# Performance work log

Hardware: AMD Instinct MI355X
Metric: run time of the kernel (lower is better)

Reference implementation:

```python
import jax, jax.numpy as jnp
import numpy as np

B, L, D_SEQ, D_GLOBAL = 32, 2048, 1024, 1024
H, DK, DV = 16, 64, 64


def setup_inputs() -> dict:
    key = jax.random.key(0)
    k1, k2, k3, k4, k5 = jax.random.split(key, 5)
    scale = 0.05
    return {
        "X": jax.random.normal(k1, (B, D_GLOBAL), dtype=jnp.float32),
        "S": jax.random.normal(k2, (B, L, D_SEQ), dtype=jnp.float32),
        "Wq": jax.random.normal(k3, (H, D_GLOBAL, DK), dtype=jnp.float32) * scale,
        "Wk": jax.random.normal(k4, (H, D_SEQ, DK), dtype=jnp.float32) * scale,
        "Wv": jax.random.normal(k5, (H, D_SEQ, DV), dtype=jnp.float32) * scale,
    }


def reference(X, S, Wq, Wk, Wv):
    # X: [B, d_global], S: [B, L, d_seq]
    d_key = Wq.shape[-1]
    inv_sqrt_dk = 1.0 / jnp.sqrt(jnp.float32(d_key))
    # Values: gelu (exact, erf-based like tf default) projection -> [B, H, L, DV]
    VS = jax.nn.gelu(jnp.einsum("bld,hdv->bhlv", S, Wv), approximate=False)
    # Single global query per head: tanh projection -> [B, H, DK]
    Q = jnp.tanh(jnp.einsum("bd,hdk->bhk", X, Wq))
    # Keys: tanh projection -> [B, H, L, DK]
    KS = jnp.tanh(jnp.einsum("bld,hdk->bhlk", S, Wk))
    # Attention logits (batched GEMV): [B, H, L]
    logits = jnp.einsum("bhk,bhlk->bhl", Q, KS) * inv_sqrt_dk
    Z = jax.nn.softmax(logits, axis=-1)
    # Weighted sum of values: [B, H, DV] -> flatten to [B, H*DV]
    Y = jnp.einsum("bhl,bhlv->bhv", Z, VS)
    return Y.reshape(Y.shape[0], -1)
```

## Files before the change

### kernel.cpp

```cpp
#include <hip/hip_runtime.h>
#include <math.h>

#define B_   32
#define L_   2048
#define DSEQ 1024
#define DGLB 1024
#define H_   16
#define DK_  64
#define DV_  64
#define LT   64
#define NT   (L_/LT)
#define PSTRIDE 66

#define WC_KSTRIDE 4096
#define WC_HSTRIDE 131072

#define AS1 __attribute__((address_space(1)))
#define AS3 __attribute__((address_space(3)))

using u16    = unsigned short;
using bf16x8 = __attribute__((ext_vector_type(8))) short;
using f32x4  = __attribute__((ext_vector_type(4))) float;

__device__ __forceinline__ u16 f2bf(float x) {
  union { float f; unsigned int u; } v; v.f = x;
  return (u16)((v.u + 0x7fffu + ((v.u >> 16) & 1u)) >> 16);
}

__device__ __forceinline__ float tanh_fast(float x) {
  float e = __builtin_exp2f(x * 2.885390081777927f);
  return 1.f - 2.f/(e + 1.f);
}

__device__ __forceinline__ float erf_fast(float x) {
  float ax = fabsf(x);
  float t  = 1.f/(1.f + 0.3275911f*ax);
  float p  = t*(0.254829592f + t*(-0.284496736f + t*(1.421413741f +
             t*(-1.453152027f + t*1.061405429f))));
  float e  = __builtin_exp2f(-ax*ax*1.4426950408889634f);
  float r  = 1.f - p*e;
  return copysignf(r, x);
}

#define PHASE_BARRIER(N)                                   \
  do {                                                     \
    __builtin_amdgcn_sched_barrier(0);                     \
    asm volatile("s_waitcnt vmcnt(" #N ")" ::: "memory");  \
    __builtin_amdgcn_s_barrier();                          \
    __builtin_amdgcn_sched_barrier(0);                     \
  } while (0)

__global__ void pack_w_kernel(const float* __restrict__ Wk,
                              const float* __restrict__ Wv,
                              u16* __restrict__ Wc) {
  const int h = blockIdx.x, j = blockIdx.y;
  const float* src = (j < DK_) ? (Wk + (size_t)h*DSEQ*DK_ + j)
                               : (Wv + (size_t)h*DSEQ*DV_ + (j - DK_));
  u16* dst = Wc + (size_t)h*WC_HSTRIDE + (size_t)j*32;
  for (int d = threadIdx.x; d < DSEQ; d += blockDim.x)
    dst[(size_t)(d >> 5)*WC_KSTRIDE + (d & 31)] = f2bf(src[(size_t)d*64]);
}

__global__ void s2bf_kernel(const float* __restrict__ S, u16* __restrict__ Sb) {
  const size_t G = (size_t)B_*L_*DSEQ/8;
  for (size_t i = (size_t)blockIdx.x*256 + threadIdx.x; i < G; i += (size_t)4096*256) {
    const float4* sp = (const float4*)(S + i*8);
    float4 v0 = sp[0], v1 = sp[1];
    bf16x8 wv;
    wv[0]=(short)f2bf(v0.x); wv[1]=(short)f2bf(v0.y);
    wv[2]=(short)f2bf(v0.z); wv[3]=(short)f2bf(v0.w);
    wv[4]=(short)f2bf(v1.x); wv[5]=(short)f2bf(v1.y);
    wv[6]=(short)f2bf(v1.z); wv[7]=(short)f2bf(v1.w);
    *(bf16x8*)(Sb + i*8) = wv;
  }
}

__global__ void q_proj_kernel(const float* __restrict__ X,
                              const float* __restrict__ Wq,
                              float* __restrict__ Q) {
  const int h = blockIdx.x, b0 = blockIdx.y*4, k = threadIdx.x;
  const float* w = Wq + (size_t)h*DGLB*DK_ + k;
  float a0=0.f, a1=0.f, a2=0.f, a3=0.f;
  for (int d = 0; d < DGLB; ++d) {
    float wv = w[(size_t)d*DK_];
    a0 += X[(size_t)(b0+0)*DGLB + d]*wv;
    a1 += X[(size_t)(b0+1)*DGLB + d]*wv;
    a2 += X[(size_t)(b0+2)*DGLB + d]*wv;
    a3 += X[(size_t)(b0+3)*DGLB + d]*wv;
  }
  Q[((size_t)(b0+0)*H_+h)*DK_+k] = tanhf(a0);
  Q[((size_t)(b0+1)*H_+h)*DK_+k] = tanhf(a1);
  Q[((size_t)(b0+2)*H_+h)*DK_+k] = tanhf(a2);
  Q[((size_t)(b0+3)*H_+h)*DK_+k] = tanhf(a3);
}

template<int BF16SRC>
__global__ __launch_bounds__(256, 3) void fused_kernel(
    const float* __restrict__ S, const u16* __restrict__ Sb,
    const u16* __restrict__ Wc, const float* __restrict__ Q,
    float* __restrict__ part) {
  __shared__ u16   Slds[3*64*128];
  __shared__ float lpart[2][64];

  const int id   = blockIdx.x;
  const int slot = id & 7;
  const int m    = id >> 3;
  const int tile = (m + (slot << 7)) & 1023;
  const int t    = tile & (NT-1), b = tile >> 5;

  const int tid  = threadIdx.x;
  const int wave = tid >> 6, lane = tid & 63;
  const int lhi  = lane >> 4, llo = lane & 15;
  const int isV  = wave & 1,  hp  = wave >> 1;
  const int h    = slot*2 + hp;

  const u16* wb = Wc + (size_t)h*WC_HSTRIDE + (size_t)(isV*64 + llo)*32 + lhi*8;
  int arow[4];
  #pragma unroll
  for (int rt = 0; rt < 4; ++rt) arow[rt] = (rt*16 + llo)*256;

  const u16*   Sv = Sb + ((size_t)b*L_ + (size_t)t*LT)*DSEQ;
  const float* Sf = S  + ((size_t)b*L_ + (size_t)t*LT)*DSEQ;

  auto stage_gl = [&](int sub) {
    const int bs = (sub % 3) * 8192;
    #pragma unroll
    for (int it = 0; it < 4; ++it) {
      const int j   = wave*4 + it;
      const int row = 4*j + (lane >> 4);
      const int g   = (lane & 15) ^ (row & 15);
      const u16* gp = Sv + (size_t)row*DSEQ + sub*128 + (g << 3);
      __builtin_amdgcn_global_load_lds(
          (const AS1 void*)gp, (AS3 void*)(Slds + bs + j*512), 16, 0, 0);
    }
  };
  auto stage_reg = [&](int sub) {
    const int bs = (sub % 3) * 16384;
    #pragma unroll
    for (int it = 0; it < 4; ++it) {
      int f = it*256 + tid, row = f >> 4, q = f & 15;
      int g = q ^ (row & 15);
      const float4* sp = (const float4*)(Sf + (size_t)row*DSEQ + sub*128 + g*8);
      float4 v0 = sp[0], v1 = sp[1];
      bf16x8 wv;
      wv[0]=(short)f2bf(v0.x); wv[1]=(short)f2bf(v0.y);
      wv[2]=(short)f2bf(v0.z); wv[3]=(short)f2bf(v0.w);
      wv[4]=(short)f2bf(v1.x); wv[5]=(short)f2bf(v1.y);
      wv[6]=(short)f2bf(v1.z); wv[7]=(short)f2bf(v1.w);
      *(bf16x8*)((char*)Slds + bs + row*256 + q*16) = wv;
    }
  };

  f32x4 acc[4][4];
  #pragma unroll
  for (int rt = 0; rt < 4; ++rt)
    #pragma unroll
    for (int c = 0; c < 4; ++c) acc[rt][c] = {0.f,0.f,0.f,0.f};

  if (BF16SRC) {
    stage_gl(0);
    stage_gl(1);
    __builtin_amdgcn_sched_barrier(0);
  }
  bf16x8 bA[4], bB[4], bC[4], bD[4];
  #pragma unroll
  for (int c = 0; c < 4; ++c) bA[c] = *(const bf16x8*)(wb + (size_t)0*WC_KSTRIDE + c*512);
  #pragma unroll
  for (int c = 0; c < 4; ++c) bB[c] = *(const bf16x8*)(wb + (size_t)1*WC_KSTRIDE + c*512);
  #pragma unroll
  for (int c = 0; c < 4; ++c) bC[c] = *(const bf16x8*)(wb + (size_t)2*WC_KSTRIDE + c*512);
  #pragma unroll
  for (int c = 0; c < 4; ++c) bD[c] = *(const bf16x8*)(wb + (size_t)3*WC_KSTRIDE + c*512);
  const u16* wbp = wb + (size_t)4*WC_KSTRIDE;
  if (BF16SRC) PHASE_BARRIER(20);

#define KSTEP(BUF, kk)                                                        \
  do {                                                                        \
    const int colb = (((kk)*4 + lhi) ^ llo) << 4;                             \
    __builtin_amdgcn_s_setprio(1);                                            \
    _Pragma("unroll")                                                         \
    for (int rt = 0; rt < 4; ++rt) {                                          \
      bf16x8 af = *(const bf16x8*)(cb + arow[rt] + colb);                     \
      acc[rt][0] = __builtin_amdgcn_mfma_f32_16x16x32_bf16(af, BUF[0], acc[rt][0], 0,0,0); \
      acc[rt][1] = __builtin_amdgcn_mfma_f32_16x16x32_bf16(af, BUF[1], acc[rt][1], 0,0,0); \
      acc[rt][2] = __builtin_amdgcn_mfma_f32_16x16x32_bf16(af, BUF[2], acc[rt][2], 0,0,0); \
      acc[rt][3] = __builtin_amdgcn_mfma_f32_16x16x32_bf16(af, BUF[3], acc[rt][3], 0,0,0); \
    }                                                                         \
    __builtin_amdgcn_s_setprio(0);                                            \
    _Pragma("unroll")                                                         \
    for (int c = 0; c < 4; ++c)                                               \
      BUF[c] = *(const bf16x8*)(wbp + c*512);                                 \
    wbp += ((s*4 + (kk) + 4) == 31) ? -(ptrdiff_t)(31*WC_KSTRIDE)             \
                                    : (ptrdiff_t)WC_KSTRIDE;                  \
  } while (0)

  #pragma unroll
  for (int s = 0; s < 8; ++s) {
    if (BF16SRC) {
      if (s < 6) { stage_gl(s + 2); __builtin_amdgcn_sched_barrier(0); }
    } else {
      stage_reg(s);
      __syncthreads();
    }
    const char* cb = (const char*)Slds + (s % 3)*16384;
    KSTEP(bA, 0); KSTEP(bB, 1); KSTEP(bC, 2); KSTEP(bD, 3);
    if (BF16SRC) {
      if (s < 6)       PHASE_BARRIER(36);
      else if (s == 6) PHASE_BARRIER(32);
    } else {
      __syncthreads();
    }
  }
#undef KSTEP

  if (!isV) {
    const float* Qb = Q + ((size_t)b*H_ + h)*DK_;
    float q[4];
    #pragma unroll
    for (int c = 0; c < 4; ++c) q[c] = Qb[16*c + llo];
    #pragma unroll
    for (int rt = 0; rt < 4; ++rt) {
      #pragma unroll
      for (int r = 0; r < 4; ++r) {
        float pl = q[0]*tanh_fast(acc[rt][0][r]) + q[1]*tanh_fast(acc[rt][1][r])
                 + q[2]*tanh_fast(acc[rt][2][r]) + q[3]*tanh_fast(acc[rt][3][r]);
        pl += __shfl_xor(pl, 1); pl += __shfl_xor(pl, 2);
        pl += __shfl_xor(pl, 4); pl += __shfl_xor(pl, 8);
        if (llo == 0) lpart[hp][rt*16 + lhi*4 + r] = pl;
      }
    }
  } else {
    #pragma unroll
    for (int rt = 0; rt < 4; ++rt)
      #pragma unroll
      for (int c = 0; c < 4; ++c)
        #pragma unroll
        for (int r = 0; r < 4; ++r) {
          float x = acc[rt][c][r];
          acc[rt][c][r] = 0.5f*x*(1.f + erf_fast(x*0.70710678118654752f));
        }
  }
  __syncthreads();

  if (isV) {
    float lg = lpart[hp][lane] * 0.125f;
    float mx = lg;
    #pragma unroll
    for (int mk = 1; mk < 64; mk <<= 1) mx = fmaxf(mx, __shfl_xor(mx, mk));
    float ev = __expf(lg - mx);
    float sv = ev;
    #pragma unroll
    for (int mk = 1; mk < 64; mk <<= 1) sv += __shfl_xor(sv, mk);

    float er[16];
    #pragma unroll
    for (int rt = 0; rt < 4; ++rt)
      #pragma unroll
      for (int r = 0; r < 4; ++r)
        er[rt*4 + r] = __shfl(ev, rt*16 + lhi*4 + r);

    float* pt = part + (((size_t)b*H_ + h)*NT + t)*PSTRIDE;
    #pragma unroll
    for (int c = 0; c < 4; ++c) {
      float y = 0.f;
      #pragma unroll
      for (int rt = 0; rt < 4; ++rt)
        #pragma unroll
        for (int r = 0; r < 4; ++r)
          y += er[rt*4 + r]*acc[rt][c][r];
      y += __shfl_xor(y, 16); y += __shfl_xor(y, 32);
      if (lhi == 0) pt[2 + 16*c + llo] = y;
    }
    if (lane == 0) { pt[0] = mx; pt[1] = sv; }
  }
}

__global__ void finalize_kernel(const float* __restrict__ part,
                                float* __restrict__ out) {
  const int h = blockIdx.x, b = blockIdx.y, v = threadIdx.x;
  const float* p = part + ((size_t)b*H_ + h)*(size_t)NT*PSTRIDE;
  float M = -3.0e38f;
  for (int tt = 0; tt < NT; ++tt) M = fmaxf(M, p[tt*PSTRIDE]);
  float ss = 0.f, y = 0.f;
  for (int tt = 0; tt < NT; ++tt) {
    float w = expf(p[tt*PSTRIDE] - M);
    ss += w*p[tt*PSTRIDE + 1];
    y  += w*p[tt*PSTRIDE + 2 + v];
  }
  out[((size_t)b*H_ + h)*DV_ + v] = y/ss;
}

extern "C" void kernel_launch(void* const* d_in, const int* in_sizes, int n_in,
                              void* d_out, int out_size, void* d_ws, size_t ws_size,
                              hipStream_t stream) {
  const float* X  = (const float*)d_in[0];
  const float* S  = (const float*)d_in[1];
  const float* Wq = (const float*)d_in[2];
  const float* Wk = (const float*)d_in[3];
  const float* Wv = (const float*)d_in[4];
  float* out = (float*)d_out;

  char* ws = (char*)d_ws;
  u16*   Wc    = (u16*)ws;
  float* Qbuf  = (float*)(ws + (4u<<20));
  float* part  = (float*)(ws + (4u<<20) + (128u<<10));
  u16*   Sb    = (u16*)(ws + (16u<<20));
  const bool useBf = ws_size >= (144ull << 20);

  pack_w_kernel  <<<dim3(H_, 128),  256, 0, stream>>>(Wk, Wv, Wc);
  q_proj_kernel  <<<dim3(H_, B_/4),  64, 0, stream>>>(X, Wq, Qbuf);
  if (useBf) {
    s2bf_kernel         <<<dim3(4096), 256, 0, stream>>>(S, Sb);
    fused_kernel<1>     <<<dim3(NT*B_*8), 256, 0, stream>>>(S, Sb, Wc, Qbuf, part);
  } else {
    fused_kernel<0>     <<<dim3(NT*B_*8), 256, 0, stream>>>(S, Sb, Wc, Qbuf, part);
  }
  finalize_kernel<<<dim3(H_, B_),    64, 0, stream>>>(part, out);
}
```

Measured before the change: 460.8 us.

## Enlarge fused GEMM tile to 128 rows with LDS-staged weights and 512 threads

The fused projection kernel now processes 128 sequence rows per block with 8 waves (two M-halves by four head/K-V column groups) instead of 64 rows with 4 waves. Weights are repacked into a new layout and staged through LDS alongside S in a triple-buffered 64-wide K pipeline, rather than streamed from global memory into registers per wave. The aim is to halve redundant weight traffic per S row and raise MFMA reuse per LDS load. In exchange the kernel uses more LDS per block, runs more barrier phases, and occupancy drops to two 512-thread blocks per CU.

```diff
diff --git a/kernel.cpp b/kernel.cpp
--- a/kernel.cpp
+++ b/kernel.cpp
@@ -8,12 +8,9 @@
 #define H_   16
 #define DK_  64
 #define DV_  64
-#define LT   64
-#define NT   (L_/LT)
+#define NT   32
 #define PSTRIDE 66
 
-#define WC_KSTRIDE 4096
-#define WC_HSTRIDE 131072
 
 #define AS1 __attribute__((address_space(1)))
 #define AS3 __attribute__((address_space(3)))
@@ -56,9 +53,11 @@
   const int h = blockIdx.x, j = blockIdx.y;
   const float* src = (j < DK_) ? (Wk + (size_t)h*DSEQ*DK_ + j)
                                : (Wv + (size_t)h*DSEQ*DV_ + (j - DK_));
-  u16* dst = Wc + (size_t)h*WC_HSTRIDE + (size_t)j*32;
-  for (int d = threadIdx.x; d < DSEQ; d += blockDim.x)
-    dst[(size_t)(d >> 5)*WC_KSTRIDE + (d & 31)] = f2bf(src[(size_t)d*64]);
+  for (int d = threadIdx.x; d < DSEQ; d += blockDim.x) {
+    int kt = d >> 6, ks = (d >> 5) & 1, lh = (d >> 3) & 3, e = d & 7;
+    Wc[(size_t)(h*128 + kt*8 + ks*4 + lh)*1024 + j*8 + e] =
+        f2bf(src[(size_t)d*64]);
+  }
 }
 
 __global__ void s2bf_kernel(const float* __restrict__ S, u16* __restrict__ Sb) {
@@ -95,59 +94,80 @@
 }
 
 template<int BF16SRC>
-__global__ __launch_bounds__(256, 3) void fused_kernel(
+__global__ __launch_bounds__(512, 2) void fused_kernel(
     const float* __restrict__ S, const u16* __restrict__ Sb,
     const u16* __restrict__ Wc, const float* __restrict__ Q,
     float* __restrict__ part) {
-  __shared__ u16   Slds[3*64*128];
-  __shared__ float lpart[2][64];
-
-  const int id   = blockIdx.x;
-  const int slot = id & 7;
-  const int m    = id >> 3;
-  const int tile = (m + (slot << 7)) & 1023;
-  const int t    = tile & (NT-1), b = tile >> 5;
+  __shared__ u16   Slds[3*24576];
+  __shared__ float lpart[2][2][64];
+
+  const int id    = blockIdx.x;
+  const int slot  = id & 7;
+  const int Mtile = ((id >> 3) + (slot << 6)) & 511;
+  const int b     = Mtile >> 4;
+  const int rowb  = (Mtile & 15) * 128;
 
   const int tid  = threadIdx.x;
   const int wave = tid >> 6, lane = tid & 63;
   const int lhi  = lane >> 4, llo = lane & 15;
-  const int isV  = wave & 1,  hp  = wave >> 1;
+  const int mw   = wave & 1,  nv  = wave >> 1;
+  const int hp   = nv >> 1,   isV = nv & 1;
   const int h    = slot*2 + hp;
 
-  const u16* wb = Wc + (size_t)h*WC_HSTRIDE + (size_t)(isV*64 + llo)*32 + lhi*8;
-  int arow[4];
-  #pragma unroll
-  for (int rt = 0; rt < 4; ++rt) arow[rt] = (rt*16 + llo)*256;
-
-  const u16*   Sv = Sb + ((size_t)b*L_ + (size_t)t*LT)*DSEQ;
-  const float* Sf = S  + ((size_t)b*L_ + (size_t)t*LT)*DSEQ;
-
-  auto stage_gl = [&](int sub) {
-    const int bs = (sub % 3) * 8192;
+  const u16* Sv = Sb + ((size_t)b*L_ + rowb)*DSEQ;
+  const float* Sf = S + ((size_t)b*L_ + rowb)*DSEQ;
+  const u16* Wh = Wc + (size_t)slot*2*131072;
+
+  auto stage_gl = [&](int sub, int p) {
+    u16* Ab = Slds + p*24576;
+    u16* Bb = Ab + 8192;
+    #pragma unroll
+    for (int it = 0; it < 2; ++it) {
+      const int j   = wave*2 + it;
+      const int row = 8*j + (lane >> 3);
+      const int g   = (lane & 7) ^ (row & 7);
+      const u16* gp = Sv + (size_t)row*DSEQ + sub*64 + g*8;
+      __builtin_amdgcn_global_load_lds(
+          (const AS1 void*)gp, (AS3 void*)(Ab + j*512), 16, 0, 0);
+    }
     #pragma unroll
     for (int it = 0; it < 4; ++it) {
-      const int j   = wave*4 + it;
-      const int row = 4*j + (lane >> 4);
-      const int g   = (lane & 15) ^ (row & 15);
-      const u16* gp = Sv + (size_t)row*DSEQ + sub*128 + (g << 3);
+      const int c  = wave*4 + it;
+      const int ks = c >> 4, lh = (c >> 2) & 3, jg = c & 3;
+      const int col = jg*64 + lane;
+      const u16* gp = Wh + (size_t)((col >> 7)*128 + sub*8 + ks*4 + lh)*1024
+                         + (size_t)(col & 127)*8;
       __builtin_amdgcn_global_load_lds(
-          (const AS1 void*)gp, (AS3 void*)(Slds + bs + j*512), 16, 0, 0);
+          (const AS1 void*)gp,
+          (AS3 void*)(Bb + ((ks*4 + lh)*256 + jg*64)*8), 16, 0, 0);
     }
   };
-  auto stage_reg = [&](int sub) {
-    const int bs = (sub % 3) * 16384;
-    #pragma unroll
-    for (int it = 0; it < 4; ++it) {
-      int f = it*256 + tid, row = f >> 4, q = f & 15;
-      int g = q ^ (row & 15);
-      const float4* sp = (const float4*)(Sf + (size_t)row*DSEQ + sub*128 + g*8);
+  auto stage_reg = [&](int sub, int p) {
+    u16* Ab = Slds + p*24576;
+    u16* Bb = Ab + 8192;
+    #pragma unroll
+    for (int it = 0; it < 2; ++it) {
+      const int j   = wave*2 + it;
+      const int row = 8*j + (lane >> 3);
+      const int g   = (lane & 7) ^ (row & 7);
+      const float4* sp = (const float4*)(Sf + (size_t)row*DSEQ + sub*64 + g*8);
       float4 v0 = sp[0], v1 = sp[1];
       bf16x8 wv;
       wv[0]=(short)f2bf(v0.x); wv[1]=(short)f2bf(v0.y);
       wv[2]=(short)f2bf(v0.z); wv[3]=(short)f2bf(v0.w);
       wv[4]=(short)f2bf(v1.x); wv[5]=(short)f2bf(v1.y);
       wv[6]=(short)f2bf(v1.z); wv[7]=(short)f2bf(v1.w);
-      *(bf16x8*)((char*)Slds + bs + row*256 + q*16) = wv;
+      *(bf16x8*)(Ab + j*512 + lane*8) = wv;
+    }
+    #pragma unroll
+    for (int it = 0; it < 4; ++it) {
+      const int c  = wave*4 + it;
+      const int ks = c >> 4, lh = (c >> 2) & 3, jg = c & 3;
+      const int col = jg*64 + lane;
+      const u16* gp = Wh + (size_t)((col >> 7)*128 + sub*8 + ks*4 + lh)*1024
+                         + (size_t)(col & 127)*8;
+      bf16x8 wv = *(const bf16x8*)gp;
+      *(bf16x8*)(Bb + ((ks*4 + lh)*256 + jg*64)*8 + lane*8) = wv;
     }
   };
 
@@ -158,60 +178,55 @@
     for (int c = 0; c < 4; ++c) acc[rt][c] = {0.f,0.f,0.f,0.f};
 
   if (BF16SRC) {
-    stage_gl(0);
-    stage_gl(1);
-    __builtin_amdgcn_sched_barrier(0);
-  }
-  bf16x8 bA[4], bB[4], bC[4], bD[4];
-  #pragma unroll
-  for (int c = 0; c < 4; ++c) bA[c] = *(const bf16x8*)(wb + (size_t)0*WC_KSTRIDE + c*512);
-  #pragma unroll
-  for (int c = 0; c < 4; ++c) bB[c] = *(const bf16x8*)(wb + (size_t)1*WC_KSTRIDE + c*512);
-  #pragma unroll
-  for (int c = 0; c < 4; ++c) bC[c] = *(const bf16x8*)(wb + (size_t)2*WC_KSTRIDE + c*512);
-  #pragma unroll
-  for (int c = 0; c < 4; ++c) bD[c] = *(const bf16x8*)(wb + (size_t)3*WC_KSTRIDE + c*512);
-  const u16* wbp = wb + (size_t)4*WC_KSTRIDE;
-  if (BF16SRC) PHASE_BARRIER(20);
-
-#define KSTEP(BUF, kk)                                                        \
-  do {                                                                        \
-    const int colb = (((kk)*4 + lhi) ^ llo) << 4;                             \
-    __builtin_amdgcn_s_setprio(1);                                            \
-    _Pragma("unroll")                                                         \
-    for (int rt = 0; rt < 4; ++rt) {                                          \
-      bf16x8 af = *(const bf16x8*)(cb + arow[rt] + colb);                     \
-      acc[rt][0] = __builtin_amdgcn_mfma_f32_16x16x32_bf16(af, BUF[0], acc[rt][0], 0,0,0); \
-      acc[rt][1] = __builtin_amdgcn_mfma_f32_16x16x32_bf16(af, BUF[1], acc[rt][1], 0,0,0); \
-      acc[rt][2] = __builtin_amdgcn_mfma_f32_16x16x32_bf16(af, BUF[2], acc[rt][2], 0,0,0); \
-      acc[rt][3] = __builtin_amdgcn_mfma_f32_16x16x32_bf16(af, BUF[3], acc[rt][3], 0,0,0); \
-    }                                                                         \
-    __builtin_amdgcn_s_setprio(0);                                            \
-    _Pragma("unroll")                                                         \
-    for (int c = 0; c < 4; ++c)                                               \
-      BUF[c] = *(const bf16x8*)(wbp + c*512);                                 \
-    wbp += ((s*4 + (kk) + 4) == 31) ? -(ptrdiff_t)(31*WC_KSTRIDE)             \
-                                    : (ptrdiff_t)WC_KSTRIDE;                  \
-  } while (0)
-
-  #pragma unroll
-  for (int s = 0; s < 8; ++s) {
+    stage_gl(0, 0);
+    stage_gl(1, 1);
+    PHASE_BARRIER(6);
+  } else {
+    stage_reg(0, 0);
+    stage_reg(1, 1);
+    __syncthreads();
+  }
+
+  const int arow0 = mw*64 + llo;
+  const int llo7  = llo & 7;
+
+  int p = 0;
+  for (int s = 0; s < 16; ++s) {
+    const int pn = (p == 2) ? 0 : p + 1;
+    const int p2 = (pn == 2) ? 0 : pn + 1;
+    if (s < 14) {
+      if (BF16SRC) { stage_gl(s + 2, p2); __builtin_amdgcn_sched_barrier(0); }
+      else         { stage_reg(s + 2, p2); }
+    }
+    const u16* Ab = Slds + p*24576;
+    const u16* Bb = Ab + 8192;
+    #pragma unroll
+    for (int kk = 0; kk < 2; ++kk) {
+      const u16* Bp = Bb + ((kk*4 + lhi)*256 + nv*64 + llo)*8;
+      bf16x8 b0 = *(const bf16x8*)(Bp);
+      bf16x8 b1 = *(const bf16x8*)(Bp + 128);
+      bf16x8 b2 = *(const bf16x8*)(Bp + 256);
+      bf16x8 b3 = *(const bf16x8*)(Bp + 384);
+      const int sl = ((kk*4 + lhi) ^ llo7)*8;
+      __builtin_amdgcn_s_setprio(1);
+      #pragma unroll
+      for (int rt = 0; rt < 4; ++rt) {
+        bf16x8 af = *(const bf16x8*)(Ab + (arow0 + rt*16)*64 + sl);
+        acc[rt][0] = __builtin_amdgcn_mfma_f32_16x16x32_bf16(af, b0, acc[rt][0], 0,0,0);
+        acc[rt][1] = __builtin_amdgcn_mfma_f32_16x16x32_bf16(af, b1, acc[rt][1], 0,0,0);
+        acc[rt][2] = __builtin_amdgcn_mfma_f32_16x16x32_bf16(af, b2, acc[rt][2], 0,0,0);
+        acc[rt][3] = __builtin_amdgcn_mfma_f32_16x16x32_bf16(af, b3, acc[rt][3], 0,0,0);
+      }
+      __builtin_amdgcn_s_setprio(0);
+    }
     if (BF16SRC) {
-      if (s < 6) { stage_gl(s + 2); __builtin_amdgcn_sched_barrier(0); }
-    } else {
-      stage_reg(s);
-      __syncthreads();
-    }
-    const char* cb = (const char*)Slds + (s % 3)*16384;
-    KSTEP(bA, 0); KSTEP(bB, 1); KSTEP(bC, 2); KSTEP(bD, 3);
-    if (BF16SRC) {
-      if (s < 6)       PHASE_BARRIER(36);
-      else if (s == 6) PHASE_BARRIER(32);
+      if (s < 14)       PHASE_BARRIER(6);
+      else if (s == 14) PHASE_BARRIER(0);
     } else {
       __syncthreads();
     }
-  }
-#undef KSTEP
+    p = pn;
+  }
 
   if (!isV) {
     const float* Qb = Q + ((size_t)b*H_ + h)*DK_;
@@ -226,7 +241,7 @@
                  + q[2]*tanh_fast(acc[rt][2][r]) + q[3]*tanh_fast(acc[rt][3][r]);
         pl += __shfl_xor(pl, 1); pl += __shfl_xor(pl, 2);
         pl += __shfl_xor(pl, 4); pl += __shfl_xor(pl, 8);
-        if (llo == 0) lpart[hp][rt*16 + lhi*4 + r] = pl;
+        if (llo == 0) lpart[mw][hp][rt*16 + lhi*4 + r] = pl;
       }
     }
   } else {
@@ -243,7 +258,7 @@
   __syncthreads();
 
   if (isV) {
-    float lg = lpart[hp][lane] * 0.125f;
+    float lg = lpart[mw][hp][lane] * 0.125f;
     float mx = lg;
     #pragma unroll
     for (int mk = 1; mk < 64; mk <<= 1) mx = fmaxf(mx, __shfl_xor(mx, mk));
@@ -259,7 +274,8 @@
       for (int r = 0; r < 4; ++r)
         er[rt*4 + r] = __shfl(ev, rt*16 + lhi*4 + r);
 
-    float* pt = part + (((size_t)b*H_ + h)*NT + t)*PSTRIDE;
+    const int t_local = (Mtile & 15)*2 + mw;
+    float* pt = part + (((size_t)b*H_ + h)*NT + t_local)*PSTRIDE;
     #pragma unroll
     for (int c = 0; c < 4; ++c) {
       float y = 0.f;
@@ -310,10 +326,10 @@
   pack_w_kernel  <<<dim3(H_, 128),  256, 0, stream>>>(Wk, Wv, Wc);
   q_proj_kernel  <<<dim3(H_, B_/4),  64, 0, stream>>>(X, Wq, Qbuf);
   if (useBf) {
-    s2bf_kernel         <<<dim3(4096), 256, 0, stream>>>(S, Sb);
-    fused_kernel<1>     <<<dim3(NT*B_*8), 256, 0, stream>>>(S, Sb, Wc, Qbuf, part);
+    s2bf_kernel       <<<dim3(4096), 256, 0, stream>>>(S, Sb);
+    fused_kernel<1>   <<<dim3(4096), 512, 0, stream>>>(S, Sb, Wc, Qbuf, part);
   } else {
-    fused_kernel<0>     <<<dim3(NT*B_*8), 256, 0, stream>>>(S, Sb, Wc, Qbuf, part);
+    fused_kernel<0>   <<<dim3(4096), 512, 0, stream>>>(S, Sb, Wc, Qbuf, part);
   }
   finalize_kernel<<<dim3(H_, B_),    64, 0, stream>>>(part, out);
 }
```

After: 621.5 us. 1.35x slower.

## Process four heads per block in two passes to halve block count

Applied to the files above, without the earlier changes.

Each block now handles four heads (two per pass) over the same S tile instead of two, so the grid shrinks from 8192 to 4096 blocks. The S tile is streamed through LDS twice, but the W prefetch and LDS pipeline continue across the pass boundary, and setup and launch overhead are amortized over more work. The intent is to cut per-block fixed costs and improve locality of the S tile in cache. The cost is a longer serial chain per block, fewer blocks to balance across CUs, and the S tile still being reloaded from global or L2 in the second pass.

```diff
diff --git a/kernel.cpp b/kernel.cpp
--- a/kernel.cpp
+++ b/kernel.cpp
@@ -104,17 +104,16 @@
 
   const int id   = blockIdx.x;
   const int slot = id & 7;
+  const int grp  = slot >> 1;
   const int m    = id >> 3;
-  const int tile = (m + (slot << 7)) & 1023;
+  const int tile = (((m + (grp << 7)) & 511) << 1) | (slot & 1);
   const int t    = tile & (NT-1), b = tile >> 5;
 
   const int tid  = threadIdx.x;
   const int wave = tid >> 6, lane = tid & 63;
   const int lhi  = lane >> 4, llo = lane & 15;
   const int isV  = wave & 1,  hp  = wave >> 1;
-  const int h    = slot*2 + hp;
-
-  const u16* wb = Wc + (size_t)h*WC_HSTRIDE + (size_t)(isV*64 + llo)*32 + lhi*8;
+
   int arow[4];
   #pragma unroll
   for (int rt = 0; rt < 4; ++rt) arow[rt] = (rt*16 + llo)*256;
@@ -124,23 +123,25 @@
 
   auto stage_gl = [&](int sub) {
     const int bs = (sub % 3) * 8192;
+    const int ko = (sub & 7) * 128;
     #pragma unroll
     for (int it = 0; it < 4; ++it) {
       const int j   = wave*4 + it;
       const int row = 4*j + (lane >> 4);
       const int g   = (lane & 15) ^ (row & 15);
-      const u16* gp = Sv + (size_t)row*DSEQ + sub*128 + (g << 3);
+      const u16* gp = Sv + (size_t)row*DSEQ + ko + (g << 3);
       __builtin_amdgcn_global_load_lds(
           (const AS1 void*)gp, (AS3 void*)(Slds + bs + j*512), 16, 0, 0);
     }
   };
   auto stage_reg = [&](int sub) {
     const int bs = (sub % 3) * 16384;
+    const int ko = (sub & 7) * 128;
     #pragma unroll
     for (int it = 0; it < 4; ++it) {
       int f = it*256 + tid, row = f >> 4, q = f & 15;
       int g = q ^ (row & 15);
-      const float4* sp = (const float4*)(Sf + (size_t)row*DSEQ + sub*128 + g*8);
+      const float4* sp = (const float4*)(Sf + (size_t)row*DSEQ + ko + g*8);
       float4 v0 = sp[0], v1 = sp[1];
       bf16x8 wv;
       wv[0]=(short)f2bf(v0.x); wv[1]=(short)f2bf(v0.y);
@@ -151,12 +152,8 @@
     }
   };
 
-  f32x4 acc[4][4];
-  #pragma unroll
-  for (int rt = 0; rt < 4; ++rt)
-    #pragma unroll
-    for (int c = 0; c < 4; ++c) acc[rt][c] = {0.f,0.f,0.f,0.f};
-
+  const u16* wb = Wc + (size_t)(grp*4 + hp)*WC_HSTRIDE
+                     + (size_t)(isV*64 + llo)*32 + lhi*8;
   if (BF16SRC) {
     stage_gl(0);
     stage_gl(1);
@@ -190,89 +187,102 @@
     _Pragma("unroll")                                                         \
     for (int c = 0; c < 4; ++c)                                               \
       BUF[c] = *(const bf16x8*)(wbp + c*512);                                 \
-    wbp += ((s*4 + (kk) + 4) == 31) ? -(ptrdiff_t)(31*WC_KSTRIDE)             \
-                                    : (ptrdiff_t)WC_KSTRIDE;                  \
+    wbp += ((s8*4 + (kk) + 4) == 31) ? wrapjump : (ptrdiff_t)WC_KSTRIDE;      \
   } while (0)
 
-  #pragma unroll
-  for (int s = 0; s < 8; ++s) {
-    if (BF16SRC) {
-      if (s < 6) { stage_gl(s + 2); __builtin_amdgcn_sched_barrier(0); }
-    } else {
-      stage_reg(s);
-      __syncthreads();
-    }
-    const char* cb = (const char*)Slds + (s % 3)*16384;
-    KSTEP(bA, 0); KSTEP(bB, 1); KSTEP(bC, 2); KSTEP(bD, 3);
-    if (BF16SRC) {
-      if (s < 6)       PHASE_BARRIER(36);
-      else if (s == 6) PHASE_BARRIER(32);
-    } else {
-      __syncthreads();
-    }
-  }
-#undef KSTEP
-
-  if (!isV) {
-    const float* Qb = Q + ((size_t)b*H_ + h)*DK_;
-    float q[4];
-    #pragma unroll
-    for (int c = 0; c < 4; ++c) q[c] = Qb[16*c + llo];
-    #pragma unroll
-    for (int rt = 0; rt < 4; ++rt) {
-      #pragma unroll
-      for (int r = 0; r < 4; ++r) {
-        float pl = q[0]*tanh_fast(acc[rt][0][r]) + q[1]*tanh_fast(acc[rt][1][r])
-                 + q[2]*tanh_fast(acc[rt][2][r]) + q[3]*tanh_fast(acc[rt][3][r]);
-        pl += __shfl_xor(pl, 1); pl += __shfl_xor(pl, 2);
-        pl += __shfl_xor(pl, 4); pl += __shfl_xor(pl, 8);
-        if (llo == 0) lpart[hp][rt*16 + lhi*4 + r] = pl;
-      }
-    }
-  } else {
+  for (int pass = 0; pass < 2; ++pass) {
+    const int h = grp*4 + pass*2 + hp;
+    const ptrdiff_t wrapjump = (pass == 0)
+        ? (ptrdiff_t)2*WC_HSTRIDE - (ptrdiff_t)31*WC_KSTRIDE
+        : -(ptrdiff_t)31*WC_KSTRIDE;
+
+    f32x4 acc[4][4];
     #pragma unroll
     for (int rt = 0; rt < 4; ++rt)
       #pragma unroll
-      for (int c = 0; c < 4; ++c)
+      for (int c = 0; c < 4; ++c) acc[rt][c] = {0.f,0.f,0.f,0.f};
+
+    #pragma unroll
+    for (int s8 = 0; s8 < 8; ++s8) {
+      const int sg = pass*8 + s8;
+      if (BF16SRC) {
+        if (sg <= 13) { stage_gl(sg + 2); __builtin_amdgcn_sched_barrier(0); }
+      } else {
+        stage_reg(sg);
+        __syncthreads();
+      }
+      const char* cb = (const char*)Slds + (sg % 3)*16384;
+      KSTEP(bA, 0); KSTEP(bB, 1); KSTEP(bC, 2); KSTEP(bD, 3);
+      if (BF16SRC) {
+        if (sg <= 13)       PHASE_BARRIER(36);
+        else if (sg == 14)  PHASE_BARRIER(32);
+      } else {
+        __syncthreads();
+      }
+    }
+
+    if (!isV) {
+      const float* Qb = Q + ((size_t)b*H_ + h)*DK_;
+      float q[4];
+      #pragma unroll
+      for (int c = 0; c < 4; ++c) q[c] = Qb[16*c + llo];
+      #pragma unroll
+      for (int rt = 0; rt < 4; ++rt) {
         #pragma unroll
         for (int r = 0; r < 4; ++r) {
-          float x = acc[rt][c][r];
-          acc[rt][c][r] = 0.5f*x*(1.f + erf_fast(x*0.70710678118654752f));
+          float pl = q[0]*tanh_fast(acc[rt][0][r]) + q[1]*tanh_fast(acc[rt][1][r])
+                   + q[2]*tanh_fast(acc[rt][2][r]) + q[3]*tanh_fast(acc[rt][3][r]);
+          pl += __shfl_xor(pl, 1); pl += __shfl_xor(pl, 2);
+          pl += __shfl_xor(pl, 4); pl += __shfl_xor(pl, 8);
+          if (llo == 0) lpart[hp][rt*16 + lhi*4 + r] = pl;
         }
-  }
-  __syncthreads();
-
-  if (isV) {
-    float lg = lpart[hp][lane] * 0.125f;
-    float mx = lg;
-    #pragma unroll
-    for (int mk = 1; mk < 64; mk <<= 1) mx = fmaxf(mx, __shfl_xor(mx, mk));
-    float ev = __expf(lg - mx);
-    float sv = ev;
-    #pragma unroll
-    for (int mk = 1; mk < 64; mk <<= 1) sv += __shfl_xor(sv, mk);
-
-    float er[16];
-    #pragma unroll
-    for (int rt = 0; rt < 4; ++rt)
-      #pragma unroll
-      for (int r = 0; r < 4; ++r)
-        er[rt*4 + r] = __shfl(ev, rt*16 + lhi*4 + r);
-
-    float* pt = part + (((size_t)b*H_ + h)*NT + t)*PSTRIDE;
-    #pragma unroll
-    for (int c = 0; c < 4; ++c) {
-      float y = 0.f;
+      }
+    } else {
+      #pragma unroll
+      for (int rt = 0; rt < 4; ++rt)
+        #pragma unroll
+        for (int c = 0; c < 4; ++c)
+          #pragma unroll
+          for (int r = 0; r < 4; ++r) {
+            float x = acc[rt][c][r];
+            acc[rt][c][r] = 0.5f*x*(1.f + erf_fast(x*0.70710678118654752f));
+          }
+    }
+    __syncthreads();
+
+    if (isV) {
+      float lg = lpart[hp][lane] * 0.125f;
+      float mx = lg;
+      #pragma unroll
+      for (int mk = 1; mk < 64; mk <<= 1) mx = fmaxf(mx, __shfl_xor(mx, mk));
+      float ev = __expf(lg - mx);
+      float sv = ev;
+      #pragma unroll
+      for (int mk = 1; mk < 64; mk <<= 1) sv += __shfl_xor(sv, mk);
+
+      float er[16];
       #pragma unroll
       for (int rt = 0; rt < 4; ++rt)
         #pragma unroll
         for (int r = 0; r < 4; ++r)
-          y += er[rt*4 + r]*acc[rt][c][r];
-      y += __shfl_xor(y, 16); y += __shfl_xor(y, 32);
-      if (lhi == 0) pt[2 + 16*c + llo] = y;
-    }
-    if (lane == 0) { pt[0] = mx; pt[1] = sv; }
-  }
+          er[rt*4 + r] = __shfl(ev, rt*16 + lhi*4 + r);
+
+      float* pt = part + (((size_t)b*H_ + h)*NT + t)*PSTRIDE;
+      #pragma unroll
+      for (int c = 0; c < 4; ++c) {
+        float y = 0.f;
+        #pragma unroll
+        for (int rt = 0; rt < 4; ++rt)
+          #pragma unroll
+          for (int r = 0; r < 4; ++r)
+            y += er[rt*4 + r]*acc[rt][c][r];
+        y += __shfl_xor(y, 16); y += __shfl_xor(y, 32);
+        if (lhi == 0) pt[2 + 16*c + llo] = y;
+      }
+      if (lane == 0) { pt[0] = mx; pt[1] = sv; }
+    }
+  }
+#undef KSTEP
 }
 
 __global__ void finalize_kernel(const float* __restrict__ part,
@@ -310,10 +320,10 @@
   pack_w_kernel  <<<dim3(H_, 128),  256, 0, stream>>>(Wk, Wv, Wc);
   q_proj_kernel  <<<dim3(H_, B_/4),  64, 0, stream>>>(X, Wq, Qbuf);
   if (useBf) {
-    s2bf_kernel         <<<dim3(4096), 256, 0, stream>>>(S, Sb);
-    fused_kernel<1>     <<<dim3(NT*B_*8), 256, 0, stream>>>(S, Sb, Wc, Qbuf, part);
+    s2bf_kernel       <<<dim3(4096), 256, 0, stream>>>(S, Sb);
+    fused_kernel<1>   <<<dim3(4096), 256, 0, stream>>>(S, Sb, Wc, Qbuf, part);
   } else {
-    fused_kernel<0>     <<<dim3(NT*B_*8), 256, 0, stream>>>(S, Sb, Wc, Qbuf, part);
+    fused_kernel<0>   <<<dim3(4096), 256, 0, stream>>>(S, Sb, Wc, Qbuf, part);
   }
   finalize_kernel<<<dim3(H_, B_),    64, 0, stream>>>(part, out);
 }
```

Measured after the change: 657.3 us. 1.43x slower.

## Retile fused kernel to one head per block with 128-row L tiles

Applied to the files above, without the earlier changes.

Changes the work split so each block handles one head over 128 sequence rows instead of two heads over 64 rows. The four waves now split the K/V output columns (32 each) and stream K in 64-wide chunks over 16 stages. Logit partial sums from two waves are combined in LDS before the softmax. The aim is to halve redundant S-tile loads per head pair and balance per-wave B-fragment loads. The cost is more pipeline stages with smaller MFMA work per stage and different register pressure.

```diff
diff --git a/kernel.cpp b/kernel.cpp
--- a/kernel.cpp
+++ b/kernel.cpp
@@ -8,8 +8,7 @@
 #define H_   16
 #define DK_  64
 #define DV_  64
-#define LT   64
-#define NT   (L_/LT)
+#define NT   32
 #define PSTRIDE 66
 
 #define WC_KSTRIDE 4096
@@ -99,141 +98,140 @@
     const float* __restrict__ S, const u16* __restrict__ Sb,
     const u16* __restrict__ Wc, const float* __restrict__ Q,
     float* __restrict__ part) {
-  __shared__ u16   Slds[3*64*128];
-  __shared__ float lpart[2][64];
+  __shared__ u16   Slds[3*8192];
+  __shared__ float lpart[2][128];
 
   const int id   = blockIdx.x;
-  const int slot = id & 7;
-  const int m    = id >> 3;
-  const int tile = (m + (slot << 7)) & 1023;
-  const int t    = tile & (NT-1), b = tile >> 5;
+  const int head = id & 15;
+  const int m    = id >> 4;
+  const int tile = (m + (head << 5)) & 511;
+  const int b    = tile >> 4, t2 = tile & 15;
 
   const int tid  = threadIdx.x;
   const int wave = tid >> 6, lane = tid & 63;
   const int lhi  = lane >> 4, llo = lane & 15;
-  const int isV  = wave & 1,  hp  = wave >> 1;
-  const int h    = slot*2 + hp;
-
-  const u16* wb = Wc + (size_t)h*WC_HSTRIDE + (size_t)(isV*64 + llo)*32 + lhi*8;
-  int arow[4];
-  #pragma unroll
-  for (int rt = 0; rt < 4; ++rt) arow[rt] = (rt*16 + llo)*256;
-
-  const u16*   Sv = Sb + ((size_t)b*L_ + (size_t)t*LT)*DSEQ;
-  const float* Sf = S  + ((size_t)b*L_ + (size_t)t*LT)*DSEQ;
+  const int llo7 = llo & 7;
+
+  int arow[8];
+  #pragma unroll
+  for (int rt = 0; rt < 8; ++rt) arow[rt] = (rt*16 + llo)*128;
+
+  const u16*   Sv = Sb + ((size_t)b*L_ + (size_t)t2*128)*DSEQ;
+  const float* Sf = S  + ((size_t)b*L_ + (size_t)t2*128)*DSEQ;
 
   auto stage_gl = [&](int sub) {
     const int bs = (sub % 3) * 8192;
+    const int ko = sub * 64;
     #pragma unroll
     for (int it = 0; it < 4; ++it) {
       const int j   = wave*4 + it;
-      const int row = 4*j + (lane >> 4);
-      const int g   = (lane & 15) ^ (row & 15);
-      const u16* gp = Sv + (size_t)row*DSEQ + sub*128 + (g << 3);
+      const int row = 8*j + (lane >> 3);
+      const int g   = (lane & 7) ^ (row & 7);
+      const u16* gp = Sv + (size_t)row*DSEQ + ko + (g << 3);
       __builtin_amdgcn_global_load_lds(
           (const AS1 void*)gp, (AS3 void*)(Slds + bs + j*512), 16, 0, 0);
     }
   };
   auto stage_reg = [&](int sub) {
     const int bs = (sub % 3) * 16384;
+    const int ko = sub * 64;
     #pragma unroll
     for (int it = 0; it < 4; ++it) {
-      int f = it*256 + tid, row = f >> 4, q = f & 15;
-      int g = q ^ (row & 15);
-      const float4* sp = (const float4*)(Sf + (size_t)row*DSEQ + sub*128 + g*8);
+      int f = it*256 + tid, row = f >> 3, q = f & 7;
+      int g = q ^ (row & 7);
+      const float4* sp = (const float4*)(Sf + (size_t)row*DSEQ + ko + g*8);
       float4 v0 = sp[0], v1 = sp[1];
       bf16x8 wv;
       wv[0]=(short)f2bf(v0.x); wv[1]=(short)f2bf(v0.y);
       wv[2]=(short)f2bf(v0.z); wv[3]=(short)f2bf(v0.w);
       wv[4]=(short)f2bf(v1.x); wv[5]=(short)f2bf(v1.y);
       wv[6]=(short)f2bf(v1.z); wv[7]=(short)f2bf(v1.w);
-      *(bf16x8*)((char*)Slds + bs + row*256 + q*16) = wv;
+      *(bf16x8*)((char*)Slds + bs + row*128 + q*16) = wv;
     }
   };
 
-  f32x4 acc[4][4];
-  #pragma unroll
-  for (int rt = 0; rt < 4; ++rt)
-    #pragma unroll
-    for (int c = 0; c < 4; ++c) acc[rt][c] = {0.f,0.f,0.f,0.f};
-
+  f32x4 acc[8][2];
+  #pragma unroll
+  for (int rt = 0; rt < 8; ++rt) {
+    acc[rt][0] = {0.f,0.f,0.f,0.f};
+    acc[rt][1] = {0.f,0.f,0.f,0.f};
+  }
+
+  const u16* wb = Wc + (size_t)head*WC_HSTRIDE
+                     + (size_t)(wave*32 + llo)*32 + lhi*8;
   if (BF16SRC) {
     stage_gl(0);
     stage_gl(1);
     __builtin_amdgcn_sched_barrier(0);
   }
-  bf16x8 bA[4], bB[4], bC[4], bD[4];
-  #pragma unroll
-  for (int c = 0; c < 4; ++c) bA[c] = *(const bf16x8*)(wb + (size_t)0*WC_KSTRIDE + c*512);
-  #pragma unroll
-  for (int c = 0; c < 4; ++c) bB[c] = *(const bf16x8*)(wb + (size_t)1*WC_KSTRIDE + c*512);
-  #pragma unroll
-  for (int c = 0; c < 4; ++c) bC[c] = *(const bf16x8*)(wb + (size_t)2*WC_KSTRIDE + c*512);
-  #pragma unroll
-  for (int c = 0; c < 4; ++c) bD[c] = *(const bf16x8*)(wb + (size_t)3*WC_KSTRIDE + c*512);
+  bf16x8 bA[2], bB[2], bC[2], bD[2];
+  #pragma unroll
+  for (int c = 0; c < 2; ++c) bA[c] = *(const bf16x8*)(wb + (size_t)0*WC_KSTRIDE + c*512);
+  #pragma unroll
+  for (int c = 0; c < 2; ++c) bB[c] = *(const bf16x8*)(wb + (size_t)1*WC_KSTRIDE + c*512);
+  #pragma unroll
+  for (int c = 0; c < 2; ++c) bC[c] = *(const bf16x8*)(wb + (size_t)2*WC_KSTRIDE + c*512);
+  #pragma unroll
+  for (int c = 0; c < 2; ++c) bD[c] = *(const bf16x8*)(wb + (size_t)3*WC_KSTRIDE + c*512);
   const u16* wbp = wb + (size_t)4*WC_KSTRIDE;
-  if (BF16SRC) PHASE_BARRIER(20);
+  if (BF16SRC) PHASE_BARRIER(12);
 
 #define KSTEP(BUF, kk)                                                        \
   do {                                                                        \
-    const int colb = (((kk)*4 + lhi) ^ llo) << 4;                             \
+    const int colb = (((kk)*4 + lhi) ^ llo7) << 4;                            \
     __builtin_amdgcn_s_setprio(1);                                            \
     _Pragma("unroll")                                                         \
-    for (int rt = 0; rt < 4; ++rt) {                                          \
+    for (int rt = 0; rt < 8; ++rt) {                                          \
       bf16x8 af = *(const bf16x8*)(cb + arow[rt] + colb);                     \
       acc[rt][0] = __builtin_amdgcn_mfma_f32_16x16x32_bf16(af, BUF[0], acc[rt][0], 0,0,0); \
       acc[rt][1] = __builtin_amdgcn_mfma_f32_16x16x32_bf16(af, BUF[1], acc[rt][1], 0,0,0); \
-      acc[rt][2] = __builtin_amdgcn_mfma_f32_16x16x32_bf16(af, BUF[2], acc[rt][2], 0,0,0); \
-      acc[rt][3] = __builtin_amdgcn_mfma_f32_16x16x32_bf16(af, BUF[3], acc[rt][3], 0,0,0); \
     }                                                                         \
     __builtin_amdgcn_s_setprio(0);                                            \
-    _Pragma("unroll")                                                         \
-    for (int c = 0; c < 4; ++c)                                               \
-      BUF[c] = *(const bf16x8*)(wbp + c*512);                                 \
-    wbp += ((s*4 + (kk) + 4) == 31) ? -(ptrdiff_t)(31*WC_KSTRIDE)             \
+    BUF[0] = *(const bf16x8*)(wbp);                                           \
+    BUF[1] = *(const bf16x8*)(wbp + 512);                                     \
+    wbp += ((s*2 + (kk) + 4) == 31) ? -(ptrdiff_t)(31*WC_KSTRIDE)             \
                                     : (ptrdiff_t)WC_KSTRIDE;                  \
   } while (0)
 
   #pragma unroll
-  for (int s = 0; s < 8; ++s) {
+  for (int s = 0; s < 16; ++s) {
     if (BF16SRC) {
-      if (s < 6) { stage_gl(s + 2); __builtin_amdgcn_sched_barrier(0); }
+      if (s <= 13) { stage_gl(s + 2); __builtin_amdgcn_sched_barrier(0); }
     } else {
       stage_reg(s);
       __syncthreads();
     }
     const char* cb = (const char*)Slds + (s % 3)*16384;
-    KSTEP(bA, 0); KSTEP(bB, 1); KSTEP(bC, 2); KSTEP(bD, 3);
+    if (s & 1) { KSTEP(bC, 0); KSTEP(bD, 1); }
+    else       { KSTEP(bA, 0); KSTEP(bB, 1); }
     if (BF16SRC) {
-      if (s < 6)       PHASE_BARRIER(36);
-      else if (s == 6) PHASE_BARRIER(32);
+      if (s <= 13)      PHASE_BARRIER(12);
+      else if (s == 14) PHASE_BARRIER(8);
     } else {
       __syncthreads();
     }
   }
 #undef KSTEP
 
-  if (!isV) {
-    const float* Qb = Q + ((size_t)b*H_ + h)*DK_;
-    float q[4];
-    #pragma unroll
-    for (int c = 0; c < 4; ++c) q[c] = Qb[16*c + llo];
-    #pragma unroll
-    for (int rt = 0; rt < 4; ++rt) {
+  if (wave < 2) {
+    const float* Qb = Q + ((size_t)b*H_ + head)*DK_;
+    float q0 = Qb[wave*32 + llo];
+    float q1 = Qb[wave*32 + 16 + llo];
+    #pragma unroll
+    for (int rt = 0; rt < 8; ++rt) {
       #pragma unroll
       for (int r = 0; r < 4; ++r) {
-        float pl = q[0]*tanh_fast(acc[rt][0][r]) + q[1]*tanh_fast(acc[rt][1][r])
-                 + q[2]*tanh_fast(acc[rt][2][r]) + q[3]*tanh_fast(acc[rt][3][r]);
+        float pl = q0*tanh_fast(acc[rt][0][r]) + q1*tanh_fast(acc[rt][1][r]);
         pl += __shfl_xor(pl, 1); pl += __shfl_xor(pl, 2);
         pl += __shfl_xor(pl, 4); pl += __shfl_xor(pl, 8);
-        if (llo == 0) lpart[hp][rt*16 + lhi*4 + r] = pl;
+        if (llo == 0) lpart[wave][rt*16 + lhi*4 + r] = pl;
       }
     }
   } else {
     #pragma unroll
-    for (int rt = 0; rt < 4; ++rt)
-      #pragma unroll
-      for (int c = 0; c < 4; ++c)
+    for (int rt = 0; rt < 8; ++rt)
+      #pragma unroll
+      for (int c = 0; c < 2; ++c)
         #pragma unroll
         for (int r = 0; r < 4; ++r) {
           float x = acc[rt][c][r];
@@ -242,36 +240,39 @@
   }
   __syncthreads();
 
-  if (isV) {
-    float lg = lpart[hp][lane] * 0.125f;
-    float mx = lg;
-    #pragma unroll
-    for (int mk = 1; mk < 64; mk <<= 1) mx = fmaxf(mx, __shfl_xor(mx, mk));
-    float ev = __expf(lg - mx);
-    float sv = ev;
-    #pragma unroll
-    for (int mk = 1; mk < 64; mk <<= 1) sv += __shfl_xor(sv, mk);
-
-    float er[16];
-    #pragma unroll
-    for (int rt = 0; rt < 4; ++rt)
-      #pragma unroll
-      for (int r = 0; r < 4; ++r)
-        er[rt*4 + r] = __shfl(ev, rt*16 + lhi*4 + r);
-
-    float* pt = part + (((size_t)b*H_ + h)*NT + t)*PSTRIDE;
-    #pragma unroll
-    for (int c = 0; c < 4; ++c) {
-      float y = 0.f;
-      #pragma unroll
-      for (int rt = 0; rt < 4; ++rt)
+  if (wave >= 2) {
+    #pragma unroll
+    for (int g = 0; g < 2; ++g) {
+      float lg = (lpart[0][g*64 + lane] + lpart[1][g*64 + lane]) * 0.125f;
+      float mx = lg;
+      #pragma unroll
+      for (int mk = 1; mk < 64; mk <<= 1) mx = fmaxf(mx, __shfl_xor(mx, mk));
+      float ev = __expf(lg - mx);
+      float sv = ev;
+      #pragma unroll
+      for (int mk = 1; mk < 64; mk <<= 1) sv += __shfl_xor(sv, mk);
+
+      float er[16];
+      #pragma unroll
+      for (int rt4 = 0; rt4 < 4; ++rt4)
         #pragma unroll
         for (int r = 0; r < 4; ++r)
-          y += er[rt*4 + r]*acc[rt][c][r];
-      y += __shfl_xor(y, 16); y += __shfl_xor(y, 32);
-      if (lhi == 0) pt[2 + 16*c + llo] = y;
-    }
-    if (lane == 0) { pt[0] = mx; pt[1] = sv; }
+          er[rt4*4 + r] = __shfl(ev, rt4*16 + lhi*4 + r);
+
+      float* pt = part + (((size_t)b*H_ + head)*NT + t2*2 + g)*PSTRIDE;
+      #pragma unroll
+      for (int c = 0; c < 2; ++c) {
+        float y = 0.f;
+        #pragma unroll
+        for (int rt4 = 0; rt4 < 4; ++rt4)
+          #pragma unroll
+          for (int r = 0; r < 4; ++r)
+            y += er[rt4*4 + r]*acc[g*4 + rt4][c][r];
+        y += __shfl_xor(y, 16); y += __shfl_xor(y, 32);
+        if (lhi == 0) pt[2 + (wave - 2)*32 + c*16 + llo] = y;
+      }
+      if (wave == 2 && lane == 0) { pt[0] = mx; pt[1] = sv; }
+    }
   }
 }
 
@@ -310,10 +311,10 @@
   pack_w_kernel  <<<dim3(H_, 128),  256, 0, stream>>>(Wk, Wv, Wc);
   q_proj_kernel  <<<dim3(H_, B_/4),  64, 0, stream>>>(X, Wq, Qbuf);
   if (useBf) {
-    s2bf_kernel         <<<dim3(4096), 256, 0, stream>>>(S, Sb);
-    fused_kernel<1>     <<<dim3(NT*B_*8), 256, 0, stream>>>(S, Sb, Wc, Qbuf, part);
+    s2bf_kernel       <<<dim3(4096), 256, 0, stream>>>(S, Sb);
+    fused_kernel<1>   <<<dim3(8192), 256, 0, stream>>>(S, Sb, Wc, Qbuf, part);
   } else {
-    fused_kernel<0>     <<<dim3(NT*B_*8), 256, 0, stream>>>(S, Sb, Wc, Qbuf, part);
+    fused_kernel<0>   <<<dim3(8192), 256, 0, stream>>>(S, Sb, Wc, Qbuf, part);
   }
   finalize_kernel<<<dim3(H_, B_),    64, 0, stream>>>(part, out);
 }
```

New measurement: 496.7 us. 1.08x slower.
